# Optimization experiments

Measured on AMD Instinct MI355X. Metric: run time of the kernel, lower is better.

## Reference

```python
import jax, jax.numpy as jnp
import numpy as np

NUM_EMBEDDINGS = 8192
EMBEDDING_DIM = 128


def setup_inputs() -> dict:
    key = jax.random.key(0)
    k1, k2 = jax.random.split(key)
    inputs = jax.random.normal(k1, (8, 32, 32, EMBEDDING_DIM), dtype=jnp.float32)
    embedding_weight = jax.random.normal(k2, (NUM_EMBEDDINGS, EMBEDDING_DIM), dtype=jnp.float32)
    return {"inputs": inputs, "embedding_weight": embedding_weight}


def reference(inputs, embedding_weight):
    # inputs: [B, H, W, C] channels-last; embedding_weight: [K, C]
    input_shape = inputs.shape
    flat_input = inputs.reshape(-1, EMBEDDING_DIM)  # [N, C]

    distances = (
        jnp.sum(flat_input ** 2, axis=1, keepdims=True)
        + jnp.sum(embedding_weight ** 2, axis=1)
        - 2.0 * flat_input @ embedding_weight.T
    )
    encoding_indices = jnp.argmin(distances, axis=1)  # [N]

    # one-hot encodings (returned by the original module)
    encodings = jax.nn.one_hot(encoding_indices, NUM_EMBEDDINGS, dtype=jnp.float32)  # [N, K]

    # quantized via direct gather (same math as one_hot @ weight, no big matmul)
    quantized = embedding_weight[encoding_indices].reshape(input_shape)  # [B,H,W,C]

    # straight-through estimator
    quantized = inputs + jax.lax.stop_gradient(quantized - inputs)

    quantized_nchw = jnp.transpose(quantized, (0, 3, 1, 2))  # [B,C,H,W]
    return quantized_nchw, encodings
```

## Files before the change

kernel.cpp:

```cpp
#include <hip/hip_runtime.h>

typedef _Float16 f16x4 __attribute__((ext_vector_type(4)));
typedef _Float16 f16x8 __attribute__((ext_vector_type(8)));
typedef float    f32x16 __attribute__((ext_vector_type(16)));
typedef float    f32x4v __attribute__((ext_vector_type(4)));

#define HN_OFF   0u
#define BEST_OFF 32768u
#define ERH_OFF  98304u
#define ERL_OFF  (98304u + 2097152u)
#define XRH_OFF  (98304u + 2u * 2097152u)
#define XRL_OFF  (98304u + 3u * 2097152u)

#define OUT_Q    0
#define OUT_ENC  1048576


__device__ __forceinline__ void gll16(const void* g, void* l) {
    __builtin_amdgcn_global_load_lds(
        (const __attribute__((address_space(1))) unsigned int*)g,
        (__attribute__((address_space(3))) unsigned int*)l, 16, 0, 0);
}

__global__ __launch_bounds__(256) void k1_convert(const float* __restrict__ x,
                                                  const float* __restrict__ e,
                                                  char* __restrict__ wsb) {
    int bx = blockIdx.x, tid = threadIdx.x;
    bool is_e = bx < 1024;
    const float* src = is_e ? e : x;
    int sec = is_e ? bx : bx - 1024;
    size_t off = (size_t)sec * 1024 + tid * 4;
    float4 v = *(const float4*)(src + off);

    f16x4 hi, lo;
    hi[0] = (_Float16)v.x; hi[1] = (_Float16)v.y;
    hi[2] = (_Float16)v.z; hi[3] = (_Float16)v.w;
    lo[0] = (_Float16)((v.x - (float)hi[0]) * 2048.0f);
    lo[1] = (_Float16)((v.y - (float)hi[1]) * 2048.0f);
    lo[2] = (_Float16)((v.z - (float)hi[2]) * 2048.0f);
    lo[3] = (_Float16)((v.w - (float)hi[3]) * 2048.0f);

    if (is_e) {
        int code = (int)(off >> 7);
        int c = (tid & 31) * 4;
        int T = code >> 6, cs = (code >> 5) & 1, colc = code & 31;
        int s = c >> 4, hf = (c >> 3) & 1;
        size_t dst = (size_t)T * 8192 + cs * 4096 + s * 512 + hf * 256
                   + colc * 8 + (c & 7);
        *(f16x4*)((_Float16*)(wsb + ERH_OFF) + dst) = hi;
        *(f16x4*)((_Float16*)(wsb + ERL_OFF) + dst) = lo;

        float ss = v.x * v.x + v.y * v.y + v.z * v.z + v.w * v.w;
        for (int o = 16; o > 0; o >>= 1) ss += __shfl_down(ss, o, 32);
        if ((tid & 31) == 0)
            ((float*)(wsb + HN_OFF))[code] = 0.5f * ss;
    } else {
        _Float16* ph = (_Float16*)(wsb + XRH_OFF);
        _Float16* pl = (_Float16*)(wsb + XRL_OFF);
        *(f16x4*)(ph + off) = hi;
        *(f16x4*)(pl + off) = lo;
        if (sec < 32)
            ((unsigned long long*)(wsb + BEST_OFF))[sec * 256 + tid] = 0ull;
    }
}

__global__ __launch_bounds__(320, 3) void k2_mfma(char* __restrict__ wsb,
                                                  float* __restrict__ out) {
    __shared__ _Float16 lds_e[2][2][8192];
    __shared__ float    lds_hn[1024];

    const _Float16* xrh = (const _Float16*)(wsb + XRH_OFF);
    const _Float16* xrl = (const _Float16*)(wsb + XRL_OFF);
    const float* hn = (const float*)(wsb + HN_OFF);
    unsigned long long* bestg = (unsigned long long*)(wsb + BEST_OFF);

    int tid = threadIdx.x;
    int lane = tid & 63, wave = tid >> 6;
    int col = lane & 31, half = lane >> 5;
    int m = blockIdx.x;
    int by = m & 7, g = m >> 3;
    int k0g = by * 1024;
    int r0 = g * 64;

    if (wave == 4) {
        f32x4v z4 = {0.f, 0.f, 0.f, 0.f};
        f32x4v* dst = (f32x4v*)(out + OUT_ENC) + (size_t)m * 16384 + lane;
        #pragma unroll 4
        for (int i = 0; i < 256; i++)
            dst[i * 64] = z4;
        return;
    }

    int rset = wave & 1, cs = wave >> 1;
    int row = r0 + rset * 32 + col;

    f16x8 xh[8], xl[8];
    #pragma unroll
    for (int s = 0; s < 8; s++) {
        xh[s] = *(const f16x8*)(xrh + (size_t)row * 128 + s * 16 + half * 8);
        xl[s] = *(const f16x8*)(xrl + (size_t)row * 128 + s * 16 + half * 8);
    }

    *(float4*)(lds_hn + tid * 4) = *(const float4*)(hn + k0g + tid * 4);

    const char* psrc = (const char*)wsb + (cs ? ERL_OFF : ERH_OFF);

    {
        const char* pb = psrc + (size_t)(by * 16) * 16384 + rset * 8192;
        char* ld = (char*)&lds_e[0][cs][0] + rset * 8192;
        #pragma unroll
        for (int j = 0; j < 8; j++)
            gll16(pb + j * 1024 + lane * 16, ld + j * 1024);
    }
    __syncthreads();

    float best = -3.0e38f;
    int bidx = 0;

    int b = 0;
    for (int t = 0; t < 16; t++) {
        if (t < 15) {
            const char* pb = psrc + (size_t)(by * 16 + t + 1) * 16384 + rset * 8192;
            char* ld = (char*)&lds_e[b ^ 1][cs][0] + rset * 8192;
            #pragma unroll
            for (int j = 0; j < 8; j++)
                gll16(pb + j * 1024 + lane * 16, ld + j * 1024);
        }

        const _Float16* Ah = &lds_e[b][0][cs * 4096 + lane * 8];
        const _Float16* Al = &lds_e[b][1][cs * 4096 + lane * 8];
        f32x16 a0, a1, a2;
        #pragma unroll
        for (int i = 0; i < 16; i++) { a0[i] = 0.f; a1[i] = 0.f; a2[i] = 0.f; }
        #pragma unroll
        for (int s = 0; s < 8; s++) {
            f16x8 eh = *(const f16x8*)(Ah + s * 512);
            f16x8 el = *(const f16x8*)(Al + s * 512);
            a0 = __builtin_amdgcn_mfma_f32_32x32x16_f16(eh, xh[s], a0, 0, 0, 0);
            a1 = __builtin_amdgcn_mfma_f32_32x32x16_f16(el, xh[s], a1, 0, 0, 0);
            a2 = __builtin_amdgcn_mfma_f32_32x32x16_f16(eh, xl[s], a2, 0, 0, 0);
        }
        int cb = k0g + t * 64 + cs * 32 + 4 * half;
        #pragma unroll
        for (int gq = 0; gq < 4; gq++) {
            float4 h4 = *(const float4*)(lds_hn + t * 64 + cs * 32 + gq * 8 + half * 4);
            #pragma unroll
            for (int j = 0; j < 4; j++) {
                int r = gq * 4 + j;
                float hv = (j == 0) ? h4.x : (j == 1) ? h4.y : (j == 2) ? h4.z : h4.w;
                float sc = a0[r] + (a1[r] + a2[r]) * (1.0f / 2048.0f) - hv;
                int cv = cb + gq * 8 + j;
                if (sc > best) { best = sc; bidx = cv; }
            }
        }

        __syncthreads();
        b ^= 1;
    }

    {
        float qs = __shfl_xor(best, 32, 64);
        int qi = __shfl_xor(bidx, 32, 64);
        if (qs > best || (qs == best && qi < bidx)) { best = qs; bidx = qi; }
        if (half == 0) {
            unsigned ub = __float_as_uint(best);
            ub = ((int)ub < 0) ? ~ub : (ub | 0x80000000u);
            unsigned long long p = ((unsigned long long)ub << 32) |
                                   (unsigned long long)(0xFFFFFFFFu - (unsigned)bidx);
            atomicMax(&bestg[row], p);
        }
    }
}

__global__ __launch_bounds__(256) void k3_final(const char* __restrict__ wsb,
                                                const float* __restrict__ wgt,
                                                float* __restrict__ out) {
    int bid = blockIdx.x;
    int n = (bid & 31) * 256 + threadIdx.x;
    int q = bid >> 5;
    unsigned long long p = ((const unsigned long long*)(wsb + BEST_OFF))[n];
    int bi = (int)(0xFFFFFFFFu - (unsigned)(p & 0xFFFFFFFFull));

    if (q == 0)
        out[(size_t)OUT_ENC + (size_t)n * 8192 + bi] = 1.0f;

    int bq = n >> 10, hw = n & 1023;
    float* o = out + (size_t)bq * 131072 + hw + (size_t)q * 32 * 1024;
    const float4* wrow = (const float4*)(wgt + (size_t)bi * 128) + q * 8;
    #pragma unroll
    for (int c4 = 0; c4 < 8; c4++) {
        float4 v = wrow[c4];
        o[(c4 * 4 + 0) * 1024] = v.x;
        o[(c4 * 4 + 1) * 1024] = v.y;
        o[(c4 * 4 + 2) * 1024] = v.z;
        o[(c4 * 4 + 3) * 1024] = v.w;
    }
}

extern "C" void kernel_launch(void* const* d_in, const int* in_sizes, int n_in,
                              void* d_out, int out_size, void* d_ws, size_t ws_size,
                              hipStream_t stream) {
    const float* x = (const float*)d_in[0];
    const float* e = (const float*)d_in[1];
    float* out = (float*)d_out;
    char* ws = (char*)d_ws;

    k1_convert<<<2048, 256, 0, stream>>>(x, e, ws);
    k2_mfma<<<1024, 320, 0, stream>>>(ws, out);
    k3_final<<<128, 256, 0, stream>>>(ws, e, out);
}
```

Before: 325.8 us.

## Drop LDS staging in distance kernel, read codebook directly from global per wave

Removes the double-buffered LDS staging of the fp16 hi/lo codebook tiles and the per-tile __syncthreads. Each of four waves now owns 32 rows and streams all 32 code tiles straight from global (L2) into registers, with the half-norms also read from global. The one-hot zero fill moves from a dedicated fifth wave into the main loop, interleaved with the MFMA work. The grid is halved to 512 blocks of 256 threads, which avoids barriers and LDS pressure but makes the four waves reload the same codebook data separately through the cache.

Result: faster. 310.9 us (-4.6%).

```diff
diff --git a/kernel.cpp b/kernel.cpp
--- a/kernel.cpp
+++ b/kernel.cpp
@@ -15,12 +15,6 @@
 #define OUT_Q    0
 #define OUT_ENC  1048576
 
-
-__device__ __forceinline__ void gll16(const void* g, void* l) {
-    __builtin_amdgcn_global_load_lds(
-        (const __attribute__((address_space(1))) unsigned int*)g,
-        (__attribute__((address_space(3))) unsigned int*)l, 16, 0, 0);
-}
 
 __global__ __launch_bounds__(256) void k1_convert(const float* __restrict__ x,
                                                   const float* __restrict__ e,
@@ -64,11 +58,8 @@
     }
 }
 
-__global__ __launch_bounds__(320, 3) void k2_mfma(char* __restrict__ wsb,
+__global__ __launch_bounds__(256, 3) void k2_mfma(char* __restrict__ wsb,
                                                   float* __restrict__ out) {
-    __shared__ _Float16 lds_e[2][2][8192];
-    __shared__ float    lds_hn[1024];
-
     const _Float16* xrh = (const _Float16*)(wsb + XRH_OFF);
     const _Float16* xrl = (const _Float16*)(wsb + XRL_OFF);
     const float* hn = (const float*)(wsb + HN_OFF);
@@ -80,19 +71,7 @@
     int m = blockIdx.x;
     int by = m & 7, g = m >> 3;
     int k0g = by * 1024;
-    int r0 = g * 64;
-
-    if (wave == 4) {
-        f32x4v z4 = {0.f, 0.f, 0.f, 0.f};
-        f32x4v* dst = (f32x4v*)(out + OUT_ENC) + (size_t)m * 16384 + lane;
-        #pragma unroll 4
-        for (int i = 0; i < 256; i++)
-            dst[i * 64] = z4;
-        return;
-    }
-
-    int rset = wave & 1, cs = wave >> 1;
-    int row = r0 + rset * 32 + col;
+    int row = g * 128 + wave * 32 + col;
 
     f16x8 xh[8], xl[8];
     #pragma unroll
@@ -101,49 +80,39 @@
         xl[s] = *(const f16x8*)(xrl + (size_t)row * 128 + s * 16 + half * 8);
     }
 
-    *(float4*)(lds_hn + tid * 4) = *(const float4*)(hn + k0g + tid * 4);
-
-    const char* psrc = (const char*)wsb + (cs ? ERL_OFF : ERH_OFF);
-
-    {
-        const char* pb = psrc + (size_t)(by * 16) * 16384 + rset * 8192;
-        char* ld = (char*)&lds_e[0][cs][0] + rset * 8192;
-        #pragma unroll
-        for (int j = 0; j < 8; j++)
-            gll16(pb + j * 1024 + lane * 16, ld + j * 1024);
-    }
-    __syncthreads();
+    size_t cbase = (size_t)by * 262144;
+    int laneoff = half * 512 + col * 16;
+    const char* ph = (const char*)wsb + ERH_OFF + cbase + laneoff;
+    const char* pl = (const char*)wsb + ERL_OFF + cbase + laneoff;
 
     float best = -3.0e38f;
     int bidx = 0;
 
-    int b = 0;
-    for (int t = 0; t < 16; t++) {
-        if (t < 15) {
-            const char* pb = psrc + (size_t)(by * 16 + t + 1) * 16384 + rset * 8192;
-            char* ld = (char*)&lds_e[b ^ 1][cs][0] + rset * 8192;
-            #pragma unroll
-            for (int j = 0; j < 8; j++)
-                gll16(pb + j * 1024 + lane * 16, ld + j * 1024);
-        }
+    f32x4v z4 = {0.f, 0.f, 0.f, 0.f};
+    f32x4v* dstf = (f32x4v*)(out + OUT_ENC) + (size_t)m * 32768 + tid;
 
-        const _Float16* Ah = &lds_e[b][0][cs * 4096 + lane * 8];
-        const _Float16* Al = &lds_e[b][1][cs * 4096 + lane * 8];
+    for (int ct = 0; ct < 32; ct++) {
+        const char* bh = ph + (size_t)ct * 8192;
+        const char* bl = pl + (size_t)ct * 8192;
         f32x16 a0, a1, a2;
         #pragma unroll
         for (int i = 0; i < 16; i++) { a0[i] = 0.f; a1[i] = 0.f; a2[i] = 0.f; }
         #pragma unroll
         for (int s = 0; s < 8; s++) {
-            f16x8 eh = *(const f16x8*)(Ah + s * 512);
-            f16x8 el = *(const f16x8*)(Al + s * 512);
+            f16x8 eh = *(const f16x8*)(bh + s * 1024);
+            f16x8 el = *(const f16x8*)(bl + s * 1024);
             a0 = __builtin_amdgcn_mfma_f32_32x32x16_f16(eh, xh[s], a0, 0, 0, 0);
             a1 = __builtin_amdgcn_mfma_f32_32x32x16_f16(el, xh[s], a1, 0, 0, 0);
             a2 = __builtin_amdgcn_mfma_f32_32x32x16_f16(eh, xl[s], a2, 0, 0, 0);
         }
-        int cb = k0g + t * 64 + cs * 32 + 4 * half;
+        #pragma unroll
+        for (int i = 0; i < 4; i++)
+            dstf[ct * 1024 + i * 256] = z4;
+
+        int cb = k0g + ct * 32 + 4 * half;
         #pragma unroll
         for (int gq = 0; gq < 4; gq++) {
-            float4 h4 = *(const float4*)(lds_hn + t * 64 + cs * 32 + gq * 8 + half * 4);
+            float4 h4 = *(const float4*)(hn + k0g + ct * 32 + gq * 8 + half * 4);
             #pragma unroll
             for (int j = 0; j < 4; j++) {
                 int r = gq * 4 + j;
@@ -153,9 +122,6 @@
                 if (sc > best) { best = sc; bidx = cv; }
             }
         }
-
-        __syncthreads();
-        b ^= 1;
     }
 
     {
@@ -206,6 +172,6 @@
     char* ws = (char*)d_ws;
 
     k1_convert<<<2048, 256, 0, stream>>>(x, e, ws);
-    k2_mfma<<<1024, 320, 0, stream>>>(ws, out);
+    k2_mfma<<<512, 256, 0, stream>>>(ws, out);
     k3_final<<<128, 256, 0, stream>>>(ws, e, out);
 }
```
